# Kernel optimization log

Hardware: AMD Instinct MI355X
Metric: run time of the kernel (lower is better)

## Reference

```python
import jax, jax.numpy as jnp
import numpy as np

B, C, H, W = 16, 256, 64, 64
K = 1024

def setup_inputs() -> dict:
    key = jax.random.key(0)
    k1, k2 = jax.random.split(key)
    x = jax.random.normal(k1, (B, C, H, W), dtype=jnp.float32)
    codebook = jax.random.normal(k2, (K, C), dtype=jnp.float32)
    return {"x": x, "codebook": codebook}


def reference(x, codebook):
    b, c, h, w = x.shape
    # (B, C, H, W) -> (B*H*W, C)
    xf = jnp.transpose(x, (0, 2, 3, 1)).reshape(-1, c)
    # Squared euclidean distances to codebook (argmin is the same as for cdist).
    x2 = jnp.sum(xf * xf, axis=-1, keepdims=True)          # (N, 1)
    c2 = jnp.sum(codebook * codebook, axis=-1)               # (K,)
    dist = x2 - 2.0 * jnp.einsum('nc,kc->nk', xf, codebook) + c2  # (N, K)
    idx = jnp.argmin(dist, axis=-1)                          # (N,)
    quant = codebook[idx]                                     # (N, C)
    commitment_loss = jnp.mean((jax.lax.stop_gradient(quant) - xf) ** 2)
    codebook_loss = jnp.mean((quant - jax.lax.stop_gradient(xf)) ** 2)
    # Straight-through estimator
    quant_out = xf + jax.lax.stop_gradient(quant - xf)
    quant_out = jnp.transpose(quant_out.reshape(b, h, w, c), (0, 3, 1, 2))
    indices = idx.reshape(b, h, w)
    return quant_out, codebook_loss, commitment_loss, indices
```

## Files before the change

kernel.cpp:

```cpp
#include <hip/hip_runtime.h>

constexpr int Bn = 16, Cd = 256, Hn = 64, Wn = 64, Kc = 1024;
constexpr int QUANT_ELEMS = Bn * Hn * Wn * Cd;
constexpr int LOSS_OFF = QUANT_ELEMS;
constexpr int IDX_OFF = QUANT_ELEMS + 2;

typedef _Float16 half8 __attribute__((ext_vector_type(8)));
typedef float f32x4 __attribute__((ext_vector_type(4)));

constexpr size_t WS_CBFH = 0;
constexpr size_t WS_CBFL = 512 * 1024;
constexpr size_t WS_C2   = 1024 * 1024;

constexpr float THR = 1e-4f;

__global__ __launch_bounds__(256) void prep(const float* __restrict__ cb,
                                            _Float16* __restrict__ cbFh,
                                            _Float16* __restrict__ cbFl,
                                            float* __restrict__ c2,
                                            float* __restrict__ out) {
    __shared__ float cbs[16][257];
    const int tid = threadIdx.x;
    const int k0 = blockIdx.x * 16;
    {
        const int c4 = (tid & 63) * 4;
        const int r0 = tid >> 6;
        #pragma unroll
        for (int it = 0; it < 4; ++it) {
            const int r = r0 + it * 4;
            const float4 v = *(const float4*)&cb[(size_t)(k0 + r) * Cd + c4];
            cbs[r][c4] = v.x; cbs[r][c4 + 1] = v.y; cbs[r][c4 + 2] = v.z; cbs[r][c4 + 3] = v.w;
        }
    }
    __syncthreads();
    {
        const int i = tid >> 4, part = tid & 15;
        float s = 0.f;
        #pragma unroll
        for (int c = part * 16; c < part * 16 + 16; ++c) { const float v = cbs[i][c]; s += v * v; }
        s += __shfl_xor(s, 1);
        s += __shfl_xor(s, 2);
        s += __shfl_xor(s, 4);
        s += __shfl_xor(s, 8);
        if (part == 0) c2[k0 + i] = s;
    }
    for (int t = tid; t < 512; t += 256) {
        const int kblk = t >> 6;
        const int l = t & 63;
        const int code_l = l & 15;
        const int cbase = kblk * 32 + (l >> 4) * 8;
        half8 hv, lv;
        #pragma unroll
        for (int j = 0; j < 8; ++j) {
            const float v = cbs[code_l][cbase + j];
            const _Float16 hh = (_Float16)v;
            hv[j] = hh;
            lv[j] = (_Float16)(v - (float)hh);
        }
        const size_t e = (size_t)(blockIdx.x * 8 + kblk) * 64 + l;
        *(half8*)(cbFh + e * 8) = hv;
        *(half8*)(cbFl + e * 8) = lv;
    }
    if (blockIdx.x == 0 && tid == 0) {
        out[LOSS_OFF] = 0.f; out[LOSS_OFF + 1] = 0.f;
    }
}

__global__ __launch_bounds__(256, 2) void vq_main(const float* __restrict__ x,
                                                  const _Float16* __restrict__ cbFh,
                                                  const _Float16* __restrict__ cbFl,
                                                  const float* __restrict__ c2,
                                                  const float* __restrict__ cb,
                                                  float* __restrict__ out) {
    __shared__ half8 Axh[2048];
    __shared__ half8 Axl[2048];
    __shared__ float q1ds[4][64];
    __shared__ int   q1is[4][64];
    __shared__ float q2ds[4][64];
    __shared__ int   q2is[4][64];
    __shared__ int   idx_s[64];
    __shared__ float red[4];
    __shared__ int   flg[64];
    __shared__ int   nflag;

    const int tid = threadIdx.x;
    const int lane = tid & 63;
    const int wv = tid >> 6;
    const int bh = blockIdx.x;
    const int b = bh >> 6, h = bh & 63;

    if (tid == 0) nflag = 0;

    {
        const int m = tid & 15;
        const int q = (tid >> 4) & 3;
        const int mt = tid >> 6;
        const int w = mt * 16 + m;
        const float* xb = x + ((size_t)b * Cd * Hn + h) * Wn + w;
        #pragma unroll
        for (int kblk = 0; kblk < 8; ++kblk) {
            half8 hv, lv;
            #pragma unroll
            for (int j = 0; j < 8; ++j) {
                const int c = kblk * 32 + q * 8 + j;
                const float v = xb[(size_t)c * (Hn * Wn)];
                const _Float16 hh = (_Float16)v;
                hv[j] = hh;
                lv[j] = (_Float16)(v - (float)hh);
            }
            const int e = (kblk * 4 + mt) * 64 + (q * 16 + m);
            Axh[e] = hv;
            Axl[e] = lv;
        }
    }
    __syncthreads();

    float q1d[16], q2d[16];
    int   q1i[16], q2i[16];
    #pragma unroll
    for (int i = 0; i < 16; ++i) { q1d[i] = 3.4e38f; q2d[i] = 3.4e38f; q1i[i] = 0; q2i[i] = 0; }

    half8 nbh[2], nbl[2];
    #pragma unroll
    for (int nt = 0; nt < 2; ++nt) {
        const int ntile = wv * 16 + nt;
        const size_t be = ((size_t)(ntile * 8) * 64 + lane) * 8;
        nbh[nt] = *(const half8*)(cbFh + be);
        nbl[nt] = *(const half8*)(cbFl + be);
    }

    #pragma unroll 1
    for (int grp = 0; grp < 8; ++grp) {
        f32x4 acc[4][2];
        #pragma unroll
        for (int mt = 0; mt < 4; ++mt) {
            acc[mt][0] = (f32x4){0.f, 0.f, 0.f, 0.f};
            acc[mt][1] = (f32x4){0.f, 0.f, 0.f, 0.f};
        }

        #pragma unroll 2
        for (int kblk = 0; kblk < 8; ++kblk) {
            const half8 cbh0 = nbh[0], cbh1 = nbh[1];
            const half8 cbl0 = nbl[0], cbl1 = nbl[1];
            {
                const int nk = (kblk + 1) & 7;
                const int ng = (grp + ((kblk + 1) >> 3)) & 7;
                #pragma unroll
                for (int nt = 0; nt < 2; ++nt) {
                    const int ntile = wv * 16 + ng * 2 + nt;
                    const size_t be = ((size_t)(ntile * 8 + nk) * 64 + lane) * 8;
                    nbh[nt] = *(const half8*)(cbFh + be);
                    nbl[nt] = *(const half8*)(cbFl + be);
                }
            }
            half8 ahf[4], alf[4];
            #pragma unroll
            for (int mt = 0; mt < 4; ++mt) {
                const int e = (kblk * 4 + mt) * 64 + lane;
                ahf[mt] = Axh[e];
                alf[mt] = Axl[e];
            }
            #pragma unroll
            for (int mt = 0; mt < 4; ++mt) {
                acc[mt][0] = __builtin_amdgcn_mfma_f32_16x16x32_f16(ahf[mt], cbh0, acc[mt][0], 0, 0, 0);
                acc[mt][1] = __builtin_amdgcn_mfma_f32_16x16x32_f16(ahf[mt], cbh1, acc[mt][1], 0, 0, 0);
            }
            #pragma unroll
            for (int mt = 0; mt < 4; ++mt) {
                acc[mt][0] = __builtin_amdgcn_mfma_f32_16x16x32_f16(ahf[mt], cbl0, acc[mt][0], 0, 0, 0);
                acc[mt][1] = __builtin_amdgcn_mfma_f32_16x16x32_f16(ahf[mt], cbl1, acc[mt][1], 0, 0, 0);
            }
            #pragma unroll
            for (int mt = 0; mt < 4; ++mt) {
                acc[mt][0] = __builtin_amdgcn_mfma_f32_16x16x32_f16(alf[mt], cbh0, acc[mt][0], 0, 0, 0);
                acc[mt][1] = __builtin_amdgcn_mfma_f32_16x16x32_f16(alf[mt], cbh1, acc[mt][1], 0, 0, 0);
            }
        }

        #pragma unroll
        for (int nt = 0; nt < 2; ++nt) {
            const int code = (wv * 16 + grp * 2 + nt) * 16 + (lane & 15);
            const float c2v = c2[code];
            #pragma unroll
            for (int mt = 0; mt < 4; ++mt) {
                #pragma unroll
                for (int reg = 0; reg < 4; ++reg) {
                    const float d = fmaf(-2.f, acc[mt][nt][reg], c2v);
                    const int qi = mt * 4 + reg;
                    const bool b1 = d < q1d[qi];
                    const bool b2 = d < q2d[qi];
                    q2d[qi] = b1 ? q1d[qi] : (b2 ? d : q2d[qi]);
                    q2i[qi] = b1 ? q1i[qi] : (b2 ? code : q2i[qi]);
                    q1d[qi] = b1 ? d : q1d[qi];
                    q1i[qi] = b1 ? code : q1i[qi];
                }
            }
        }
    }

    #pragma unroll
    for (int off = 1; off < 16; off <<= 1) {
        #pragma unroll
        for (int qi = 0; qi < 16; ++qi) {
            const float od1 = __shfl_xor(q1d[qi], off);
            const int   oi1 = __shfl_xor(q1i[qi], off);
            const float od2 = __shfl_xor(q2d[qi], off);
            const int   oi2 = __shfl_xor(q2i[qi], off);
            const bool ob = od1 < q1d[qi];
            const float ld = ob ? q1d[qi] : od1;
            const int   li = ob ? q1i[qi] : oi1;
            const bool o2 = od2 < q2d[qi];
            const float md = o2 ? od2 : q2d[qi];
            const int   mi = o2 ? oi2 : q2i[qi];
            const bool lb = ld < md;
            q2d[qi] = lb ? ld : md;
            q2i[qi] = lb ? li : mi;
            q1d[qi] = ob ? od1 : q1d[qi];
            q1i[qi] = ob ? oi1 : q1i[qi];
        }
    }
    if ((lane & 15) == 0) {
        #pragma unroll
        for (int qi = 0; qi < 16; ++qi) {
            const int mt = qi >> 2, reg = qi & 3;
            const int row = mt * 16 + (lane >> 4) * 4 + reg;
            q1ds[wv][row] = q1d[qi];
            q1is[wv][row] = q1i[qi];
            q2ds[wv][row] = q2d[qi];
            q2is[wv][row] = q2i[qi];
        }
    }
    __syncthreads();
    if (tid < 64) {
        float d1 = q1ds[0][tid]; int i1 = q1is[0][tid];
        float d2 = q2ds[0][tid]; int i2 = q2is[0][tid];
        #pragma unroll
        for (int v = 1; v < 4; ++v) {
            const float od1 = q1ds[v][tid]; const int oi1 = q1is[v][tid];
            const float od2 = q2ds[v][tid]; const int oi2 = q2is[v][tid];
            const bool ob = od1 < d1;
            const float ld = ob ? d1 : od1;
            const int   li = ob ? i1 : oi1;
            const bool o2 = od2 < d2;
            const float md = o2 ? od2 : d2;
            const int   mi = o2 ? oi2 : i2;
            const bool lb = ld < md;
            d2 = lb ? ld : md;
            i2 = lb ? li : mi;
            d1 = ob ? od1 : d1;
            i1 = ob ? oi1 : i1;
        }
        idx_s[tid] = i1;
        if (d2 - d1 < THR) {
            const int pos = atomicAdd(&nflag, 1);
            flg[pos] = tid | (i2 << 6);
        }
    }
    __syncthreads();

    const int nf = nflag;
    for (int fi = 0; fi < nf; ++fi) {
        if (wv == 0) {
            const int pack = flg[fi];
            const int w = pack & 63;
            const int i2 = pack >> 6;
            const int i1 = idx_s[w];
            const int mt = w >> 4, m = w & 15;
            float s1 = 0.f, s2 = 0.f;
            #pragma unroll
            for (int cc = 0; cc < 4; ++cc) {
                const int c = lane * 4 + cc;
                const int kblk = c >> 5, q = (c >> 3) & 3, j = c & 7;
                const int e = (kblk * 4 + mt) * 64 + q * 16 + m;
                const float xv = (float)Axh[e][j] + (float)Axl[e][j];
                const float e1 = cb[(size_t)i1 * Cd + c] - xv;
                const float e2 = cb[(size_t)i2 * Cd + c] - xv;
                s1 = fmaf(e1, e1, s1);
                s2 = fmaf(e2, e2, s2);
            }
            #pragma unroll
            for (int off = 32; off >= 1; off >>= 1) {
                s1 += __shfl_xor(s1, off);
                s2 += __shfl_xor(s2, off);
            }
            if (lane == 0 && (s2 < s1 || (s2 == s1 && i2 < i1))) idx_s[w] = i2;
        }
    }
    __syncthreads();

    if (tid < 64) out[IDX_OFF + bh * 64 + tid] = (float)idx_s[tid];

    {
        const int w = tid & 63;
        const int cq = wv;
        const int m = w & 15, mt = w >> 4;
        const int myidx = idx_s[w];
        const float4* cbrow = (const float4*)(cb + (size_t)myidx * Cd + cq * 64);
        float lsum = 0.f;
        #pragma unroll
        for (int half = 0; half < 2; ++half) {
            const int kblk = cq * 2 + half;
            #pragma unroll
            for (int q = 0; q < 4; ++q) {
                const int e = (kblk * 4 + mt) * 64 + q * 16 + m;
                const half8 hv = Axh[e];
                const half8 lv = Axl[e];
                const float4 qa = cbrow[half * 8 + q * 2];
                const float4 qb = cbrow[half * 8 + q * 2 + 1];
                const float qv[8] = {qa.x, qa.y, qa.z, qa.w, qb.x, qb.y, qb.z, qb.w};
                const int cbase = cq * 64 + half * 32 + q * 8;
                #pragma unroll
                for (int j = 0; j < 8; ++j) {
                    const float xv = (float)hv[j] + (float)lv[j];
                    const float dd = qv[j] - xv;
                    lsum += dd * dd;
                    out[(((size_t)b * Cd + cbase + j) * Hn + h) * Wn + w] = qv[j];
                }
            }
        }
        #pragma unroll
        for (int off = 32; off >= 1; off >>= 1) lsum += __shfl_xor(lsum, off);
        if (lane == 0) red[wv] = lsum;
    }
    __syncthreads();
    if (tid == 0) {
        const float s = (red[0] + red[1] + red[2] + red[3]) * (1.0f / 16777216.0f);
        atomicAdd(out + LOSS_OFF, s);
        atomicAdd(out + LOSS_OFF + 1, s);
    }
}

extern "C" void kernel_launch(void* const* d_in, const int* in_sizes, int n_in,
                              void* d_out, int out_size, void* d_ws, size_t ws_size,
                              hipStream_t stream) {
    const float* x  = (const float*)d_in[0];
    const float* cb = (const float*)d_in[1];
    float* out = (float*)d_out;
    char* ws = (char*)d_ws;
    _Float16* cbFh = (_Float16*)(ws + WS_CBFH);
    _Float16* cbFl = (_Float16*)(ws + WS_CBFL);
    float* c2      = (float*)(ws + WS_C2);

    prep<<<64, 256, 0, stream>>>(cb, cbFh, cbFl, c2, out);
    vq_main<<<Bn * Hn, 256, 0, stream>>>(x, cbFh, cbFl, c2, cb, out);
}
```

Before: 242.1 us.

## Split each block's work across eight waves instead of four

Doubles the block size to 512 threads. Each wave now covers half the 64 pixel rows (two m-tiles) for one quarter of the codebook, which halves the per-wave accumulators and top-2 state. The aim is more waves in flight per CU to hide codebook load latency and the MFMA dependency chains. The cost is that each codebook fragment is now loaded by two waves instead of one, plus an extra cross-wave merge step through shared memory. The x staging and the output/loss epilogue are also redistributed over the eight waves.

```diff
diff --git a/kernel.cpp b/kernel.cpp
--- a/kernel.cpp
+++ b/kernel.cpp
@@ -66,7 +66,7 @@
     }
 }
 
-__global__ __launch_bounds__(256, 2) void vq_main(const float* __restrict__ x,
+__global__ __launch_bounds__(512, 4) void vq_main(const float* __restrict__ x,
                                                   const _Float16* __restrict__ cbFh,
                                                   const _Float16* __restrict__ cbFl,
                                                   const float* __restrict__ c2,
@@ -74,18 +74,20 @@
                                                   float* __restrict__ out) {
     __shared__ half8 Axh[2048];
     __shared__ half8 Axl[2048];
-    __shared__ float q1ds[4][64];
-    __shared__ int   q1is[4][64];
-    __shared__ float q2ds[4][64];
-    __shared__ int   q2is[4][64];
+    __shared__ float q1ds[8][32];
+    __shared__ int   q1is[8][32];
+    __shared__ float q2ds[8][32];
+    __shared__ int   q2is[8][32];
     __shared__ int   idx_s[64];
-    __shared__ float red[4];
+    __shared__ float red[8];
     __shared__ int   flg[64];
     __shared__ int   nflag;
 
     const int tid = threadIdx.x;
     const int lane = tid & 63;
     const int wv = tid >> 6;
+    const int mth = wv & 1;
+    const int ntq = wv >> 1;
     const int bh = blockIdx.x;
     const int b = bh >> 6, h = bh & 63;
 
@@ -94,11 +96,13 @@
     {
         const int m = tid & 15;
         const int q = (tid >> 4) & 3;
-        const int mt = tid >> 6;
-        const int w = mt * 16 + m;
+        const int mtg = (tid >> 6) & 3;
+        const int kh = tid >> 8;
+        const int w = mtg * 16 + m;
         const float* xb = x + ((size_t)b * Cd * Hn + h) * Wn + w;
         #pragma unroll
-        for (int kblk = 0; kblk < 8; ++kblk) {
+        for (int kk = 0; kk < 4; ++kk) {
+            const int kblk = kh * 4 + kk;
             half8 hv, lv;
             #pragma unroll
             for (int j = 0; j < 8; ++j) {
@@ -108,22 +112,22 @@
                 hv[j] = hh;
                 lv[j] = (_Float16)(v - (float)hh);
             }
-            const int e = (kblk * 4 + mt) * 64 + (q * 16 + m);
+            const int e = (kblk * 4 + mtg) * 64 + (q * 16 + m);
             Axh[e] = hv;
             Axl[e] = lv;
         }
     }
     __syncthreads();
 
-    float q1d[16], q2d[16];
-    int   q1i[16], q2i[16];
+    float q1d[8], q2d[8];
+    int   q1i[8], q2i[8];
     #pragma unroll
-    for (int i = 0; i < 16; ++i) { q1d[i] = 3.4e38f; q2d[i] = 3.4e38f; q1i[i] = 0; q2i[i] = 0; }
+    for (int i = 0; i < 8; ++i) { q1d[i] = 3.4e38f; q2d[i] = 3.4e38f; q1i[i] = 0; q2i[i] = 0; }
 
     half8 nbh[2], nbl[2];
     #pragma unroll
     for (int nt = 0; nt < 2; ++nt) {
-        const int ntile = wv * 16 + nt;
+        const int ntile = ntq * 16 + nt;
         const size_t be = ((size_t)(ntile * 8) * 64 + lane) * 8;
         nbh[nt] = *(const half8*)(cbFh + be);
         nbl[nt] = *(const half8*)(cbFl + be);
@@ -131,12 +135,11 @@
 
     #pragma unroll 1
     for (int grp = 0; grp < 8; ++grp) {
-        f32x4 acc[4][2];
-        #pragma unroll
-        for (int mt = 0; mt < 4; ++mt) {
-            acc[mt][0] = (f32x4){0.f, 0.f, 0.f, 0.f};
-            acc[mt][1] = (f32x4){0.f, 0.f, 0.f, 0.f};
-        }
+        f32x4 acc[2][2];
+        acc[0][0] = (f32x4){0.f, 0.f, 0.f, 0.f};
+        acc[0][1] = (f32x4){0.f, 0.f, 0.f, 0.f};
+        acc[1][0] = (f32x4){0.f, 0.f, 0.f, 0.f};
+        acc[1][1] = (f32x4){0.f, 0.f, 0.f, 0.f};
 
         #pragma unroll 2
         for (int kblk = 0; kblk < 8; ++kblk) {
@@ -147,46 +150,46 @@
                 const int ng = (grp + ((kblk + 1) >> 3)) & 7;
                 #pragma unroll
                 for (int nt = 0; nt < 2; ++nt) {
-                    const int ntile = wv * 16 + ng * 2 + nt;
+                    const int ntile = ntq * 16 + ng * 2 + nt;
                     const size_t be = ((size_t)(ntile * 8 + nk) * 64 + lane) * 8;
                     nbh[nt] = *(const half8*)(cbFh + be);
                     nbl[nt] = *(const half8*)(cbFl + be);
                 }
             }
-            half8 ahf[4], alf[4];
-            #pragma unroll
-            for (int mt = 0; mt < 4; ++mt) {
-                const int e = (kblk * 4 + mt) * 64 + lane;
-                ahf[mt] = Axh[e];
-                alf[mt] = Axl[e];
-            }
-            #pragma unroll
-            for (int mt = 0; mt < 4; ++mt) {
-                acc[mt][0] = __builtin_amdgcn_mfma_f32_16x16x32_f16(ahf[mt], cbh0, acc[mt][0], 0, 0, 0);
-                acc[mt][1] = __builtin_amdgcn_mfma_f32_16x16x32_f16(ahf[mt], cbh1, acc[mt][1], 0, 0, 0);
-            }
-            #pragma unroll
-            for (int mt = 0; mt < 4; ++mt) {
-                acc[mt][0] = __builtin_amdgcn_mfma_f32_16x16x32_f16(ahf[mt], cbl0, acc[mt][0], 0, 0, 0);
-                acc[mt][1] = __builtin_amdgcn_mfma_f32_16x16x32_f16(ahf[mt], cbl1, acc[mt][1], 0, 0, 0);
-            }
-            #pragma unroll
-            for (int mt = 0; mt < 4; ++mt) {
-                acc[mt][0] = __builtin_amdgcn_mfma_f32_16x16x32_f16(alf[mt], cbh0, acc[mt][0], 0, 0, 0);
-                acc[mt][1] = __builtin_amdgcn_mfma_f32_16x16x32_f16(alf[mt], cbh1, acc[mt][1], 0, 0, 0);
+            half8 ahf[2], alf[2];
+            #pragma unroll
+            for (int ml = 0; ml < 2; ++ml) {
+                const int e = (kblk * 4 + mth * 2 + ml) * 64 + lane;
+                ahf[ml] = Axh[e];
+                alf[ml] = Axl[e];
+            }
+            #pragma unroll
+            for (int ml = 0; ml < 2; ++ml) {
+                acc[ml][0] = __builtin_amdgcn_mfma_f32_16x16x32_f16(ahf[ml], cbh0, acc[ml][0], 0, 0, 0);
+                acc[ml][1] = __builtin_amdgcn_mfma_f32_16x16x32_f16(ahf[ml], cbh1, acc[ml][1], 0, 0, 0);
+            }
+            #pragma unroll
+            for (int ml = 0; ml < 2; ++ml) {
+                acc[ml][0] = __builtin_amdgcn_mfma_f32_16x16x32_f16(ahf[ml], cbl0, acc[ml][0], 0, 0, 0);
+                acc[ml][1] = __builtin_amdgcn_mfma_f32_16x16x32_f16(ahf[ml], cbl1, acc[ml][1], 0, 0, 0);
+            }
+            #pragma unroll
+            for (int ml = 0; ml < 2; ++ml) {
+                acc[ml][0] = __builtin_amdgcn_mfma_f32_16x16x32_f16(alf[ml], cbh0, acc[ml][0], 0, 0, 0);
+                acc[ml][1] = __builtin_amdgcn_mfma_f32_16x16x32_f16(alf[ml], cbh1, acc[ml][1], 0, 0, 0);
             }
         }
 
         #pragma unroll
         for (int nt = 0; nt < 2; ++nt) {
-            const int code = (wv * 16 + grp * 2 + nt) * 16 + (lane & 15);
+            const int code = (ntq * 16 + grp * 2 + nt) * 16 + (lane & 15);
             const float c2v = c2[code];
             #pragma unroll
-            for (int mt = 0; mt < 4; ++mt) {
+            for (int ml = 0; ml < 2; ++ml) {
                 #pragma unroll
                 for (int reg = 0; reg < 4; ++reg) {
-                    const float d = fmaf(-2.f, acc[mt][nt][reg], c2v);
-                    const int qi = mt * 4 + reg;
+                    const float d = fmaf(-2.f, acc[ml][nt][reg], c2v);
+                    const int qi = ml * 4 + reg;
                     const bool b1 = d < q1d[qi];
                     const bool b2 = d < q2d[qi];
                     q2d[qi] = b1 ? q1d[qi] : (b2 ? d : q2d[qi]);
@@ -201,7 +204,7 @@
     #pragma unroll
     for (int off = 1; off < 16; off <<= 1) {
         #pragma unroll
-        for (int qi = 0; qi < 16; ++qi) {
+        for (int qi = 0; qi < 8; ++qi) {
             const float od1 = __shfl_xor(q1d[qi], off);
             const int   oi1 = __shfl_xor(q1i[qi], off);
             const float od2 = __shfl_xor(q2d[qi], off);
@@ -221,23 +224,25 @@
     }
     if ((lane & 15) == 0) {
         #pragma unroll
-        for (int qi = 0; qi < 16; ++qi) {
-            const int mt = qi >> 2, reg = qi & 3;
-            const int row = mt * 16 + (lane >> 4) * 4 + reg;
-            q1ds[wv][row] = q1d[qi];
-            q1is[wv][row] = q1i[qi];
-            q2ds[wv][row] = q2d[qi];
-            q2is[wv][row] = q2i[qi];
+        for (int qi = 0; qi < 8; ++qi) {
+            const int ml = qi >> 2, reg = qi & 3;
+            const int rl = ml * 16 + (lane >> 4) * 4 + reg;
+            q1ds[wv][rl] = q1d[qi];
+            q1is[wv][rl] = q1i[qi];
+            q2ds[wv][rl] = q2d[qi];
+            q2is[wv][rl] = q2i[qi];
         }
     }
     __syncthreads();
     if (tid < 64) {
-        float d1 = q1ds[0][tid]; int i1 = q1is[0][tid];
-        float d2 = q2ds[0][tid]; int i2 = q2is[0][tid];
+        const int hh = tid >> 5, rl = tid & 31;
+        float d1 = q1ds[hh][rl]; int i1 = q1is[hh][rl];
+        float d2 = q2ds[hh][rl]; int i2 = q2is[hh][rl];
         #pragma unroll
         for (int v = 1; v < 4; ++v) {
-            const float od1 = q1ds[v][tid]; const int oi1 = q1is[v][tid];
-            const float od2 = q2ds[v][tid]; const int oi2 = q2is[v][tid];
+            const int w2 = hh + 2 * v;
+            const float od1 = q1ds[w2][rl]; const int oi1 = q1is[w2][rl];
+            const float od2 = q2ds[w2][rl]; const int oi2 = q2is[w2][rl];
             const bool ob = od1 < d1;
             const float ld = ob ? d1 : od1;
             const int   li = ob ? i1 : oi1;
@@ -266,13 +271,15 @@
             const int i2 = pack >> 6;
             const int i1 = idx_s[w];
             const int mt = w >> 4, m = w & 15;
+            const _Float16* axh = (const _Float16*)Axh;
+            const _Float16* axl = (const _Float16*)Axl;
             float s1 = 0.f, s2 = 0.f;
             #pragma unroll
             for (int cc = 0; cc < 4; ++cc) {
                 const int c = lane * 4 + cc;
                 const int kblk = c >> 5, q = (c >> 3) & 3, j = c & 7;
-                const int e = (kblk * 4 + mt) * 64 + q * 16 + m;
-                const float xv = (float)Axh[e][j] + (float)Axl[e][j];
+                const int e8 = ((kblk * 4 + mt) * 64 + q * 16 + m) * 8 + j;
+                const float xv = (float)axh[e8] + (float)axl[e8];
                 const float e1 = cb[(size_t)i1 * Cd + c] - xv;
                 const float e2 = cb[(size_t)i2 * Cd + c] - xv;
                 s1 = fmaf(e1, e1, s1);
@@ -292,30 +299,26 @@
 
     {
         const int w = tid & 63;
-        const int cq = wv;
+        const int kblk = wv;
         const int m = w & 15, mt = w >> 4;
         const int myidx = idx_s[w];
-        const float4* cbrow = (const float4*)(cb + (size_t)myidx * Cd + cq * 64);
+        const float4* cbrow = (const float4*)(cb + (size_t)myidx * Cd + kblk * 32);
         float lsum = 0.f;
         #pragma unroll
-        for (int half = 0; half < 2; ++half) {
-            const int kblk = cq * 2 + half;
-            #pragma unroll
-            for (int q = 0; q < 4; ++q) {
-                const int e = (kblk * 4 + mt) * 64 + q * 16 + m;
-                const half8 hv = Axh[e];
-                const half8 lv = Axl[e];
-                const float4 qa = cbrow[half * 8 + q * 2];
-                const float4 qb = cbrow[half * 8 + q * 2 + 1];
-                const float qv[8] = {qa.x, qa.y, qa.z, qa.w, qb.x, qb.y, qb.z, qb.w};
-                const int cbase = cq * 64 + half * 32 + q * 8;
-                #pragma unroll
-                for (int j = 0; j < 8; ++j) {
-                    const float xv = (float)hv[j] + (float)lv[j];
-                    const float dd = qv[j] - xv;
-                    lsum += dd * dd;
-                    out[(((size_t)b * Cd + cbase + j) * Hn + h) * Wn + w] = qv[j];
-                }
+        for (int q = 0; q < 4; ++q) {
+            const int e = (kblk * 4 + mt) * 64 + q * 16 + m;
+            const half8 hv = Axh[e];
+            const half8 lv = Axl[e];
+            const float4 qa = cbrow[q * 2];
+            const float4 qb = cbrow[q * 2 + 1];
+            const float qv[8] = {qa.x, qa.y, qa.z, qa.w, qb.x, qb.y, qb.z, qb.w};
+            const int cbase = kblk * 32 + q * 8;
+            #pragma unroll
+            for (int j = 0; j < 8; ++j) {
+                const float xv = (float)hv[j] + (float)lv[j];
+                const float dd = qv[j] - xv;
+                lsum += dd * dd;
+                out[(((size_t)b * Cd + cbase + j) * Hn + h) * Wn + w] = qv[j];
             }
         }
         #pragma unroll
@@ -324,7 +327,10 @@
     }
     __syncthreads();
     if (tid == 0) {
-        const float s = (red[0] + red[1] + red[2] + red[3]) * (1.0f / 16777216.0f);
+        float s = 0.f;
+        #pragma unroll
+        for (int i = 0; i < 8; ++i) s += red[i];
+        s *= (1.0f / 16777216.0f);
         atomicAdd(out + LOSS_OFF, s);
         atomicAdd(out + LOSS_OFF + 1, s);
     }
@@ -342,5 +348,5 @@
     float* c2      = (float*)(ws + WS_C2);
 
     prep<<<64, 256, 0, stream>>>(cb, cbFh, cbFl, c2, out);
-    vq_main<<<Bn * Hn, 256, 0, stream>>>(x, cbFh, cbFl, c2, cb, out);
+    vq_main<<<Bn * Hn, 512, 0, stream>>>(x, cbFh, cbFl, c2, cb, out);
 }
```

Result: faster. 225.7 us (-6.8%).
